# Kernel optimization log

Hardware: AMD Instinct MI355X
Metric: run time of the kernel (lower is better)

Reference implementation:

```python
import jax, jax.numpy as jnp
import numpy as np
import math

B, H, T, DH, D = 1, 8, 2048, 64, 64
NEG_INF = -1e30
EPS = 1e-9

def setup_inputs() -> dict:
    key = jax.random.key(0)
    ks = jax.random.split(key, 6)
    q = jax.random.normal(ks[0], (B, H, T, DH), dtype=jnp.float32)
    k = jax.random.normal(ks[1], (B, H, T, DH), dtype=jnp.float32)
    v = jax.random.normal(ks[2], (B, H, T, DH), dtype=jnp.float32)
    edge_type_bias = 0.1 * jax.random.normal(ks[3], (4,), dtype=jnp.float32)
    neigh_idx = jax.random.randint(ks[4], (H, T, D), 0, T).astype(jnp.int32)
    edge_type = jax.random.randint(ks[5], (H, T, D), 0, 5).astype(jnp.int32)
    return {"q": q, "k": k, "v": v, "edge_type_bias": edge_type_bias,
            "neigh_idx": neigh_idx, "edge_type": edge_type}

def _masked_softmax(scores, mask):
    # scores: [B,H,T,D] fp32, mask: [1,H,T,D] bool; zeros on all-masked rows
    masked = jnp.where(mask, scores, NEG_INF)
    m = jnp.max(masked, axis=-1, keepdims=True)
    e = jnp.where(mask, jnp.exp(masked - m), 0.0)
    denom = jnp.maximum(jnp.sum(e, axis=-1, keepdims=True), EPS)
    return e / denom

def reference(q, k, v, edge_type_bias, neigh_idx, edge_type):
    Bq, Hq, Tq, dh = q.shape
    # safe_neighbor_idx: clamp to valid range
    s_idx = jnp.clip(neigh_idx, 0, Tq - 1)                       # [H,T,D]
    # causal_neighbor_mask: valid (>=0) and neighbor <= query position
    pos = jnp.arange(Tq, dtype=neigh_idx.dtype)[None, :, None]    # [1,T,1]
    mask = (neigh_idx >= 0) & (neigh_idx <= pos)                  # [H,T,D]
    # edge-type bias: type 0 -> no bias, types 1..4 -> learnable bias
    full_bias = jnp.concatenate([jnp.zeros((1,), jnp.float32),
                                 edge_type_bias.astype(jnp.float32)])
    bias_htd = full_bias[edge_type]                               # [H,T,D]
    # gather neighbor K/V: k_g[b,h,t,n,:] = k[b,h,s_idx[h,t,n],:]
    h_ix = jnp.arange(Hq)[:, None, None]                          # [H,1,1]
    k_g = k[:, h_ix, s_idx]                                       # [B,H,T,D,dh]
    v_g = v[:, h_ix, s_idx]                                       # [B,H,T,D,dh]
    scores = jnp.einsum('bhtc,bhtnc->bhtn',
                        q.astype(jnp.float32),
                        k_g.astype(jnp.float32)) / math.sqrt(dh)
    scores = scores + bias_htd[None]                              # [B,H,T,D]
    w = _masked_softmax(scores, mask[None])                       # [B,H,T,D]
    y = jnp.einsum('bhtn,bhtnc->bhtc', w, v_g.astype(jnp.float32))
    return y.astype(v.dtype)
```

## Files before the change

kernel.cpp:

```cpp
#include <hip/hip_runtime.h>
#include <hip/hip_fp16.h>

constexpr int H  = 8;
constexpr int T  = 2048;
constexpr int DH = 64;
constexpr int D  = 64;
constexpr int NKV = H * T * DH;

typedef _Float16 half2v __attribute__((ext_vector_type(2)));

#if defined(__has_builtin)
#if __has_builtin(__builtin_amdgcn_fdot2)
#define HAVE_FDOT2 1
#endif
#endif

__device__ __forceinline__ float dot2acc(half2v a, half2v b, float c) {
#ifdef HAVE_FDOT2
    return __builtin_amdgcn_fdot2(a, b, c, false);
#else
    return c + (float)a.x * (float)b.x + (float)a.y * (float)b.y;
#endif
}

__device__ __forceinline__ half2v h2add(half2v a, int braw) {
    half2v b = __builtin_bit_cast(half2v, braw);
    return a + b;
}

__device__ __forceinline__ half2v f2h2(float x, float y) {
    __half2 h = __float22half2_rn(make_float2(x, y));
    return __builtin_bit_cast(half2v, h);
}

__global__ __launch_bounds__(256) void cvt_f32_f16(
    const float* __restrict__ k, const float* __restrict__ v,
    __half* __restrict__ kh, __half* __restrict__ vh)
{
    const int i = (blockIdx.x * 256 + threadIdx.x) * 8;
    const float* src = (blockIdx.y == 0) ? k : v;
    __half*      dst = (blockIdx.y == 0) ? kh : vh;
    const float4 a = *reinterpret_cast<const float4*>(src + i);
    const float4 b = *reinterpret_cast<const float4*>(src + i + 4);
    __half2 hh[4];
    hh[0] = __float22half2_rn(make_float2(a.x, a.y));
    hh[1] = __float22half2_rn(make_float2(a.z, a.w));
    hh[2] = __float22half2_rn(make_float2(b.x, b.y));
    hh[3] = __float22half2_rn(make_float2(b.z, b.w));
    *reinterpret_cast<float4*>(dst + i) = *reinterpret_cast<const float4*>(hh);
}

__global__ __launch_bounds__(256) void wayfinder_attn_f16(
    const float* __restrict__ q,
    const __half* __restrict__ kh,
    const __half* __restrict__ vh,
    const float* __restrict__ eb,
    const int*   __restrict__ nidx,
    const int*   __restrict__ etyp,
    float* __restrict__ out)
{
    const int wave = threadIdx.x >> 6;
    const int lane = threadIdx.x & 63;
    const int bid  = blockIdx.x;
    const int work = ((bid & 7) << 9) | (bid >> 3);
    const int flat = (work << 2) + wave;
    const int h    = flat >> 11;
    const int t    = flat & (T - 1);
    const int grp  = lane >> 3;
    const int sub  = lane & 7;

    const long long rowoff = (long long)flat * DH;
    const int*      nrow   = nidx + (long long)flat * D;
    const int*      erow   = etyp + (long long)flat * D;

    int idx_i[8], et_i[8];
    #pragma unroll
    for (int i = 0; i < 8; ++i) idx_i[i] = nrow[i * 8 + grp];
    #pragma unroll
    for (int i = 0; i < 8; ++i) et_i[i]  = erow[i * 8 + grp];

    const float4 qa = *reinterpret_cast<const float4*>(q + rowoff + sub * 8);
    const float4 qb = *reinterpret_cast<const float4*>(q + rowoff + sub * 8 + 4);
    half2v qp[4];
    qp[0] = f2h2(qa.x, qa.y);
    qp[1] = f2h2(qa.z, qa.w);
    qp[2] = f2h2(qb.x, qb.y);
    qp[3] = f2h2(qb.z, qb.w);

    const __half* khead = kh + (long long)h * T * DH;
    const __half* vhead = vh + (long long)h * T * DH;

    float4 kf[8], vf[8];
    #pragma unroll
    for (int i = 0; i < 8; ++i) {
        const int s = min(max(idx_i[i], 0), T - 1);
        const long long ro = (long long)s * DH + sub * 8;
        kf[i] = *reinterpret_cast<const float4*>(khead + ro);
        vf[i] = *reinterpret_cast<const float4*>(vhead + ro);
    }

    const float4 ebv = *reinterpret_cast<const float4*>(eb);

    float sc[8];
    #pragma unroll
    for (int i = 0; i < 8; ++i) {
        const half2v* kp = reinterpret_cast<const half2v*>(&kf[i]);
        float p = dot2acc(qp[0], kp[0],
                  dot2acc(qp[1], kp[1],
                  dot2acc(qp[2], kp[2],
                  dot2acc(qp[3], kp[3], 0.0f))));
        p += __shfl_xor(p, 1);
        p += __shfl_xor(p, 2);
        p += __shfl_xor(p, 4);
        sc[i] = p;
    }

    bool  msk[8];
    float masked[8];
    float mx = -1e30f;
    #pragma unroll
    for (int i = 0; i < 8; ++i) {
        const int et = et_i[i];
        const float bias = (et == 1) ? ebv.x : (et == 2) ? ebv.y :
                           (et == 3) ? ebv.z : (et == 4) ? ebv.w : 0.0f;
        msk[i]    = (idx_i[i] >= 0) && (idx_i[i] <= t);
        masked[i] = msk[i] ? fmaf(sc[i], 0.125f, bias) : -1e30f;
        mx = fmaxf(mx, masked[i]);
    }
    mx = fmaxf(mx, __shfl_xor(mx, 8));
    mx = fmaxf(mx, __shfl_xor(mx, 16));
    mx = fmaxf(mx, __shfl_xor(mx, 32));

    float e[8];
    float sum = 0.0f;
    #pragma unroll
    for (int i = 0; i < 8; ++i) {
        e[i] = msk[i] ? __expf(masked[i] - mx) : 0.0f;
        sum += e[i];
    }
    sum += __shfl_xor(sum, 8);
    sum += __shfl_xor(sum, 16);
    sum += __shfl_xor(sum, 32);
    const float rden = 1.0f / fmaxf(sum, 1e-9f);

    float acc[8] = {0.f, 0.f, 0.f, 0.f, 0.f, 0.f, 0.f, 0.f};
    #pragma unroll
    for (int i = 0; i < 8; ++i) {
        const float w = e[i] * rden;
        const half2v* vp = reinterpret_cast<const half2v*>(&vf[i]);
        acc[0] += w * (float)vp[0].x;  acc[1] += w * (float)vp[0].y;
        acc[2] += w * (float)vp[1].x;  acc[3] += w * (float)vp[1].y;
        acc[4] += w * (float)vp[2].x;  acc[5] += w * (float)vp[2].y;
        acc[6] += w * (float)vp[3].x;  acc[7] += w * (float)vp[3].y;
    }

    half2v h0 = f2h2(acc[0], acc[1]);
    half2v h1 = f2h2(acc[2], acc[3]);
    half2v h2 = f2h2(acc[4], acc[5]);
    half2v h3 = f2h2(acc[6], acc[7]);
    #pragma unroll
    for (int off = 8; off <= 32; off <<= 1) {
        h0 = h2add(h0, __shfl_xor(__builtin_bit_cast(int, h0), off));
        h1 = h2add(h1, __shfl_xor(__builtin_bit_cast(int, h1), off));
        h2 = h2add(h2, __shfl_xor(__builtin_bit_cast(int, h2), off));
        h3 = h2add(h3, __shfl_xor(__builtin_bit_cast(int, h3), off));
    }

    if (lane < 16) {
        const int s8   = (lane & 7) * 8;
        const int half = lane >> 3;
        const float4 o = half
            ? make_float4((float)h2.x, (float)h2.y, (float)h3.x, (float)h3.y)
            : make_float4((float)h0.x, (float)h0.y, (float)h1.x, (float)h1.y);
        *reinterpret_cast<float4*>(out + rowoff + s8 + half * 4) = o;
    }
}

__global__ __launch_bounds__(256) void wayfinder_attn_f32(
    const float* __restrict__ q, const float* __restrict__ k,
    const float* __restrict__ v, const float* __restrict__ eb,
    const int* __restrict__ nidx, const int* __restrict__ etyp,
    float* __restrict__ out)
{
    const int wave = threadIdx.x >> 6;
    const int lane = threadIdx.x & 63;
    const int flat = (blockIdx.x << 2) + wave;
    const int h    = flat >> 11;
    const int t    = flat & (T - 1);
    const int grp  = lane >> 4;
    const int sub  = lane & 15;

    __shared__ int    sidx[4][64];
    __shared__ float  ssc [4][64];
    __shared__ float2 swv [4][64];

    const long long rowoff = (long long)flat * DH;
    const long long noff = (long long)flat * D + lane;
    const int  idx = nidx[noff];
    const int  et  = etyp[noff];
    const int  s   = min(max(idx, 0), T - 1);
    const bool msk = (idx >= 0) && (idx <= t);
    const float4 ebv  = *reinterpret_cast<const float4*>(eb);
    const float  bias = (et == 1) ? ebv.x : (et == 2) ? ebv.y :
                        (et == 3) ? ebv.z : (et == 4) ? ebv.w : 0.0f;
    sidx[wave][lane] = s;
    const float4 qf = *reinterpret_cast<const float4*>(q + rowoff + sub * 4);
    __syncthreads();

    const float* khead = k + (long long)h * T * DH;
    #pragma unroll
    for (int i = 0; i < 16; ++i) {
        const int n  = i * 4 + grp;
        const int sn = sidx[wave][n];
        const float4 kf = *reinterpret_cast<const float4*>(khead + sn * DH + sub * 4);
        float p = qf.x * kf.x + qf.y * kf.y + qf.z * kf.z + qf.w * kf.w;
        p += __shfl_xor(p, 1);
        p += __shfl_xor(p, 2);
        p += __shfl_xor(p, 4);
        p += __shfl_xor(p, 8);
        if (sub == 0) ssc[wave][n] = p;
    }
    __syncthreads();

    const float sc     = ssc[wave][lane];
    const float masked = msk ? (sc * 0.125f + bias) : -1e30f;
    float mx = masked;
    #pragma unroll
    for (int off = 32; off > 0; off >>= 1) mx = fmaxf(mx, __shfl_xor(mx, off));
    const float e = msk ? __expf(masked - mx) : 0.0f;
    float sum = e;
    #pragma unroll
    for (int off = 32; off > 0; off >>= 1) sum += __shfl_xor(sum, off);
    const float w = e / fmaxf(sum, 1e-9f);
    swv[wave][lane] = make_float2(w, __int_as_float(s));
    __syncthreads();

    const float* vhead = v + (long long)h * T * DH;
    float4 acc = make_float4(0.f, 0.f, 0.f, 0.f);
    #pragma unroll
    for (int i = 0; i < 16; ++i) {
        const int    n  = i * 4 + grp;
        const float2 ws = swv[wave][n];
        const int    sn = __float_as_int(ws.y);
        const float4 vf = *reinterpret_cast<const float4*>(vhead + sn * DH + sub * 4);
        acc.x += ws.x * vf.x; acc.y += ws.x * vf.y;
        acc.z += ws.x * vf.z; acc.w += ws.x * vf.w;
    }
    #pragma unroll
    for (int off = 16; off <= 32; off <<= 1) {
        acc.x += __shfl_xor(acc.x, off); acc.y += __shfl_xor(acc.y, off);
        acc.z += __shfl_xor(acc.z, off); acc.w += __shfl_xor(acc.w, off);
    }
    if (lane < 16)
        *reinterpret_cast<float4*>(out + rowoff + sub * 4) = acc;
}

extern "C" void kernel_launch(void* const* d_in, const int* in_sizes, int n_in,
                              void* d_out, int out_size, void* d_ws, size_t ws_size,
                              hipStream_t stream) {
    const float* q    = (const float*)d_in[0];
    const float* k    = (const float*)d_in[1];
    const float* v    = (const float*)d_in[2];
    const float* eb   = (const float*)d_in[3];
    const int*   nidx = (const int*)d_in[4];
    const int*   etyp = (const int*)d_in[5];
    float* out = (float*)d_out;

    const size_t need = (size_t)2 * NKV * sizeof(__half);
    if (ws_size >= need) {
        __half* kh = (__half*)d_ws;
        __half* vh = kh + NKV;
        dim3 cgrid(NKV / (256 * 8), 2);
        hipLaunchKernelGGL(cvt_f32_f16, cgrid, dim3(256), 0, stream, k, v, kh, vh);
        hipLaunchKernelGGL(wayfinder_attn_f16, dim3(H * T / 4), dim3(256), 0, stream,
                           q, kh, vh, eb, nidx, etyp, out);
    } else {
        hipLaunchKernelGGL(wayfinder_attn_f32, dim3(H * T / 4), dim3(256), 0, stream,
                           q, k, v, eb, nidx, etyp, out);
    }
}
```

Baseline: 25.47 us.

## Stage V gathers through async global-to-LDS loads and use permlane swaps for reductions

V rows are no longer gathered into registers. They are fetched with asynchronous global_load_lds into a per-wave shared buffer, which cuts register pressure so the kernel can request 5 blocks per SM. Neighbor index and edge-type loads become vectorized int4 reads, and mask and bias are computed up front. The xor-16 and xor-32 cross-lane reductions now use permlane16/32 swap builtins instead of generic shuffles. The trade-off is 32KB of LDS per block, which limits occupancy. Correctness also depends on the swap builtin returning the own and partner values as assumed.

```diff
diff --git a/kernel.cpp b/kernel.cpp
--- a/kernel.cpp
+++ b/kernel.cpp
@@ -13,6 +13,12 @@
 #if __has_builtin(__builtin_amdgcn_fdot2)
 #define HAVE_FDOT2 1
 #endif
+#if __has_builtin(__builtin_amdgcn_permlane32_swap)
+#define HAVE_PL32 1
+#endif
+#if __has_builtin(__builtin_amdgcn_permlane16_swap)
+#define HAVE_PL16 1
+#endif
 #endif
 
 __device__ __forceinline__ float dot2acc(half2v a, half2v b, float c) {
@@ -23,14 +29,69 @@
 #endif
 }
 
-__device__ __forceinline__ half2v h2add(half2v a, int braw) {
-    half2v b = __builtin_bit_cast(half2v, braw);
-    return a + b;
-}
+__device__ __forceinline__ half2v h2bits(int b) { return __builtin_bit_cast(half2v, b); }
 
 __device__ __forceinline__ half2v f2h2(float x, float y) {
     __half2 h = __float22half2_rn(make_float2(x, y));
     return __builtin_bit_cast(half2v, h);
+}
+
+__device__ __forceinline__ float xor32add_f(float x) {
+#ifdef HAVE_PL32
+    unsigned u = __builtin_bit_cast(unsigned, x);
+    auto r = __builtin_amdgcn_permlane32_swap(u, u, false, false);
+    return __builtin_bit_cast(float, (unsigned)r[0]) + __builtin_bit_cast(float, (unsigned)r[1]);
+#else
+    return x + __shfl_xor(x, 32);
+#endif
+}
+__device__ __forceinline__ float xor32max_f(float x) {
+#ifdef HAVE_PL32
+    unsigned u = __builtin_bit_cast(unsigned, x);
+    auto r = __builtin_amdgcn_permlane32_swap(u, u, false, false);
+    return fmaxf(__builtin_bit_cast(float, (unsigned)r[0]), __builtin_bit_cast(float, (unsigned)r[1]));
+#else
+    return fmaxf(x, __shfl_xor(x, 32));
+#endif
+}
+__device__ __forceinline__ float xor16add_f(float x) {
+#ifdef HAVE_PL16
+    unsigned u = __builtin_bit_cast(unsigned, x);
+    auto r = __builtin_amdgcn_permlane16_swap(u, u, false, false);
+    return __builtin_bit_cast(float, (unsigned)r[0]) + __builtin_bit_cast(float, (unsigned)r[1]);
+#else
+    return x + __shfl_xor(x, 16);
+#endif
+}
+__device__ __forceinline__ float xor16max_f(float x) {
+#ifdef HAVE_PL16
+    unsigned u = __builtin_bit_cast(unsigned, x);
+    auto r = __builtin_amdgcn_permlane16_swap(u, u, false, false);
+    return fmaxf(__builtin_bit_cast(float, (unsigned)r[0]), __builtin_bit_cast(float, (unsigned)r[1]));
+#else
+    return fmaxf(x, __shfl_xor(x, 16));
+#endif
+}
+__device__ __forceinline__ half2v xor32add_h2(half2v x) {
+#ifdef HAVE_PL32
+    unsigned u = __builtin_bit_cast(unsigned, x);
+    auto r = __builtin_amdgcn_permlane32_swap(u, u, false, false);
+    return h2bits((int)r[0]) + h2bits((int)r[1]);
+#else
+    return x + h2bits(__shfl_xor(__builtin_bit_cast(int, x), 32));
+#endif
+}
+__device__ __forceinline__ half2v xor16add_h2(half2v x) {
+#ifdef HAVE_PL16
+    unsigned u = __builtin_bit_cast(unsigned, x);
+    auto r = __builtin_amdgcn_permlane16_swap(u, u, false, false);
+    return h2bits((int)r[0]) + h2bits((int)r[1]);
+#else
+    return x + h2bits(__shfl_xor(__builtin_bit_cast(int, x), 16));
+#endif
+}
+__device__ __forceinline__ half2v xor8add_h2(half2v x) {
+    return x + h2bits(__shfl_xor(__builtin_bit_cast(int, x), 8));
 }
 
 __global__ __launch_bounds__(256) void cvt_f32_f16(
@@ -50,7 +111,7 @@
     *reinterpret_cast<float4*>(dst + i) = *reinterpret_cast<const float4*>(hh);
 }
 
-__global__ __launch_bounds__(256) void wayfinder_attn_f16(
+__global__ __launch_bounds__(256, 5) void wayfinder_attn_f16(
     const float* __restrict__ q,
     const __half* __restrict__ kh,
     const __half* __restrict__ vh,
@@ -59,6 +120,8 @@
     const int*   __restrict__ etyp,
     float* __restrict__ out)
 {
+    __shared__ __half vlds[4][8][512];
+
     const int wave = threadIdx.x >> 6;
     const int lane = threadIdx.x & 63;
     const int bid  = blockIdx.x;
@@ -73,33 +136,56 @@
     const int*      nrow   = nidx + (long long)flat * D;
     const int*      erow   = etyp + (long long)flat * D;
 
-    int idx_i[8], et_i[8];
-    #pragma unroll
-    for (int i = 0; i < 8; ++i) idx_i[i] = nrow[i * 8 + grp];
-    #pragma unroll
-    for (int i = 0; i < 8; ++i) et_i[i]  = erow[i * 8 + grp];
+    const int4 i0 = *reinterpret_cast<const int4*>(nrow + grp * 8);
+    const int4 i1 = *reinterpret_cast<const int4*>(nrow + grp * 8 + 4);
+    const int4 e0 = *reinterpret_cast<const int4*>(erow + grp * 8);
+    const int4 e1 = *reinterpret_cast<const int4*>(erow + grp * 8 + 4);
 
     const float4 qa = *reinterpret_cast<const float4*>(q + rowoff + sub * 8);
     const float4 qb = *reinterpret_cast<const float4*>(q + rowoff + sub * 8 + 4);
+
+    const int idx_i[8] = {i0.x, i0.y, i0.z, i0.w, i1.x, i1.y, i1.z, i1.w};
+    const int et_i [8] = {e0.x, e0.y, e0.z, e0.w, e1.x, e1.y, e1.z, e1.w};
+
+    const __half* khead = kh + (long long)h * T * DH;
+    const __half* vhead = vh + (long long)h * T * DH;
+
+    int s_i[8];
+    int mskbits = 0;
+    #pragma unroll
+    for (int i = 0; i < 8; ++i) {
+        s_i[i] = min(max(idx_i[i], 0), T - 1);
+        mskbits |= ((idx_i[i] >= 0) && (idx_i[i] <= t)) ? (1 << i) : 0;
+    }
+
+    float4 kf[8];
+    #pragma unroll
+    for (int i = 0; i < 8; ++i)
+        kf[i] = *reinterpret_cast<const float4*>(khead + (long long)s_i[i] * DH + sub * 8);
+
+    #pragma unroll
+    for (int i = 0; i < 8; ++i) {
+        const __half* src = vhead + (long long)s_i[i] * DH + sub * 8;
+        __builtin_amdgcn_global_load_lds(
+            (const __attribute__((address_space(1))) void*)src,
+            (__attribute__((address_space(3))) void*)(&vlds[wave][i][0]),
+            16, 0, 0);
+    }
+
+    const float4 ebv = *reinterpret_cast<const float4*>(eb);
+    float bias_i[8];
+    #pragma unroll
+    for (int i = 0; i < 8; ++i) {
+        const int et = et_i[i];
+        bias_i[i] = (et == 1) ? ebv.x : (et == 2) ? ebv.y :
+                    (et == 3) ? ebv.z : (et == 4) ? ebv.w : 0.0f;
+    }
+
     half2v qp[4];
     qp[0] = f2h2(qa.x, qa.y);
     qp[1] = f2h2(qa.z, qa.w);
     qp[2] = f2h2(qb.x, qb.y);
     qp[3] = f2h2(qb.z, qb.w);
-
-    const __half* khead = kh + (long long)h * T * DH;
-    const __half* vhead = vh + (long long)h * T * DH;
-
-    float4 kf[8], vf[8];
-    #pragma unroll
-    for (int i = 0; i < 8; ++i) {
-        const int s = min(max(idx_i[i], 0), T - 1);
-        const long long ro = (long long)s * DH + sub * 8;
-        kf[i] = *reinterpret_cast<const float4*>(khead + ro);
-        vf[i] = *reinterpret_cast<const float4*>(vhead + ro);
-    }
-
-    const float4 ebv = *reinterpret_cast<const float4*>(eb);
 
     float sc[8];
     #pragma unroll
@@ -115,39 +201,39 @@
         sc[i] = p;
     }
 
-    bool  msk[8];
     float masked[8];
     float mx = -1e30f;
     #pragma unroll
     for (int i = 0; i < 8; ++i) {
-        const int et = et_i[i];
-        const float bias = (et == 1) ? ebv.x : (et == 2) ? ebv.y :
-                           (et == 3) ? ebv.z : (et == 4) ? ebv.w : 0.0f;
-        msk[i]    = (idx_i[i] >= 0) && (idx_i[i] <= t);
-        masked[i] = msk[i] ? fmaf(sc[i], 0.125f, bias) : -1e30f;
+        const bool mk = (mskbits >> i) & 1;
+        masked[i] = mk ? fmaf(sc[i], 0.125f, bias_i[i]) : -1e30f;
         mx = fmaxf(mx, masked[i]);
     }
     mx = fmaxf(mx, __shfl_xor(mx, 8));
-    mx = fmaxf(mx, __shfl_xor(mx, 16));
-    mx = fmaxf(mx, __shfl_xor(mx, 32));
+    mx = xor16max_f(mx);
+    mx = xor32max_f(mx);
 
     float e[8];
     float sum = 0.0f;
     #pragma unroll
     for (int i = 0; i < 8; ++i) {
-        e[i] = msk[i] ? __expf(masked[i] - mx) : 0.0f;
+        const bool mk = (mskbits >> i) & 1;
+        e[i] = mk ? __expf(masked[i] - mx) : 0.0f;
         sum += e[i];
     }
     sum += __shfl_xor(sum, 8);
-    sum += __shfl_xor(sum, 16);
-    sum += __shfl_xor(sum, 32);
+    sum = xor16add_f(sum);
+    sum = xor32add_f(sum);
     const float rden = 1.0f / fmaxf(sum, 1e-9f);
 
+    asm volatile("s_waitcnt vmcnt(0)" ::: "memory");
+
     float acc[8] = {0.f, 0.f, 0.f, 0.f, 0.f, 0.f, 0.f, 0.f};
     #pragma unroll
     for (int i = 0; i < 8; ++i) {
         const float w = e[i] * rden;
-        const half2v* vp = reinterpret_cast<const half2v*>(&vf[i]);
+        const float4 vfi = *reinterpret_cast<const float4*>(&vlds[wave][i][lane * 8]);
+        const half2v* vp = reinterpret_cast<const half2v*>(&vfi);
         acc[0] += w * (float)vp[0].x;  acc[1] += w * (float)vp[0].y;
         acc[2] += w * (float)vp[1].x;  acc[3] += w * (float)vp[1].y;
         acc[4] += w * (float)vp[2].x;  acc[5] += w * (float)vp[2].y;
@@ -158,13 +244,12 @@
     half2v h1 = f2h2(acc[2], acc[3]);
     half2v h2 = f2h2(acc[4], acc[5]);
     half2v h3 = f2h2(acc[6], acc[7]);
-    #pragma unroll
-    for (int off = 8; off <= 32; off <<= 1) {
-        h0 = h2add(h0, __shfl_xor(__builtin_bit_cast(int, h0), off));
-        h1 = h2add(h1, __shfl_xor(__builtin_bit_cast(int, h1), off));
-        h2 = h2add(h2, __shfl_xor(__builtin_bit_cast(int, h2), off));
-        h3 = h2add(h3, __shfl_xor(__builtin_bit_cast(int, h3), off));
-    }
+    h0 = xor8add_h2(h0);  h1 = xor8add_h2(h1);
+    h2 = xor8add_h2(h2);  h3 = xor8add_h2(h3);
+    h0 = xor16add_h2(h0); h1 = xor16add_h2(h1);
+    h2 = xor16add_h2(h2); h3 = xor16add_h2(h3);
+    h0 = xor32add_h2(h0); h1 = xor32add_h2(h1);
+    h2 = xor32add_h2(h2); h3 = xor32add_h2(h3);
 
     if (lane < 16) {
         const int s8   = (lane & 7) * 8;
```

After: 29.55 us. 16.0% more time.
